# Kernel optimization log

Hardware: AMD Instinct MI355X
Metric: run time of the kernel (lower is better)

## Reference

```python
import jax, jax.numpy as jnp
import numpy as np

D_MODEL = 1472
N_HEADS = 6
D_KV = 64
INNER = N_HEADS * D_KV
NUM_BUCKETS = 32
MAX_DIST = 128


def _relative_position_bucket(relative_position, bidirectional=True,
                              num_buckets=NUM_BUCKETS, max_distance=MAX_DIST):
    ret = jnp.zeros_like(relative_position)
    if bidirectional:
        num_buckets //= 2
        ret = ret + (relative_position > 0).astype(jnp.int32) * num_buckets
        rel = jnp.abs(relative_position)
    else:
        rel = -jnp.minimum(relative_position, 0)
    max_exact = num_buckets // 2
    is_small = rel < max_exact
    rel_f = jnp.maximum(rel, 1).astype(jnp.float32)
    large = max_exact + (
        jnp.log(rel_f / max_exact) / np.log(max_distance / max_exact)
        * (num_buckets - max_exact)
    ).astype(jnp.int32)
    large = jnp.minimum(large, num_buckets - 1)
    return ret + jnp.where(is_small, rel, large)


def _position_bias(q_len, k_len, rel_bias):
    # rel_bias: [num_buckets, n_heads]
    ctx = jnp.arange(q_len)[:, None]
    mem = jnp.arange(k_len)[None, :]
    buckets = _relative_position_bucket(mem - ctx, bidirectional=True)
    values = rel_bias[buckets]                 # [Q, K, H]
    return jnp.transpose(values, (2, 0, 1))[None]  # [1, H, Q, K]


def setup_inputs() -> dict:
    key = jax.random.key(0)
    ks = jax.random.split(key, 8)
    B, S = 4, 2048
    scale = 0.02
    return {
        "kv_sequences": jax.random.normal(ks[0], (B, S, D_MODEL), jnp.float32),
        "q_sequences": jax.random.normal(ks[1], (B, S, D_MODEL), jnp.float32),
        "mask": jnp.zeros((B, 1, S, S), jnp.float32),
        "WQ": jax.random.normal(ks[2], (D_MODEL, INNER), jnp.float32) * scale,
        "WK": jax.random.normal(ks[3], (D_MODEL, INNER), jnp.float32) * scale,
        "WV": jax.random.normal(ks[4], (D_MODEL, INNER), jnp.float32) * scale,
        "WO": jax.random.normal(ks[5], (INNER, D_MODEL), jnp.float32) * scale,
        "rel_bias": jax.random.normal(ks[6], (NUM_BUCKETS, N_HEADS), jnp.float32) * scale,
    }


def reference(kv_sequences, q_sequences, mask, WQ, WK, WV, WO, rel_bias):
    B, Kl, _ = kv_sequences.shape
    Ql = q_sequences.shape[1]
    # projections -> [B, H, L, d_kv]
    q = (q_sequences @ WQ).reshape(B, Ql, N_HEADS, D_KV).transpose(0, 2, 1, 3)
    k = (kv_sequences @ WK).reshape(B, Kl, N_HEADS, D_KV).transpose(0, 2, 1, 3)
    v = (kv_sequences @ WV).reshape(B, Kl, N_HEADS, D_KV).transpose(0, 2, 1, 3)
    # T5-style: no 1/sqrt(d) scaling
    logits = jnp.einsum("bhqd,bhkd->bhqk", q, k)
    logits = logits + _position_bias(Ql, Kl, rel_bias)
    logits = logits + mask
    attn = jax.nn.softmax(logits.astype(jnp.float32), axis=-1).astype(logits.dtype)
    out = jnp.einsum("bhqk,bhkd->bhqd", attn, v)
    out = out.transpose(0, 2, 1, 3).reshape(B, Ql, INNER)
    return out @ WO
```

## Files before the change

### kernel.cpp

```cpp
#include <hip/hip_runtime.h>
#include <hip/hip_fp16.h>
#include <cstdint>

#define DM    1472
#define NH    6
#define DKV   64
#define INNER 384
#define BATCH 4
#define SEQ   2048
#define LOG2E 1.4426950408889634f

typedef __attribute__((ext_vector_type(8))) _Float16 half8;
typedef __attribute__((ext_vector_type(4))) _Float16 half4;
typedef __attribute__((ext_vector_type(4))) float f32x4;

__device__ __forceinline__ int swz64(int row, int b)  { return b ^ (((row >> 1) & 3) << 4); }
__device__ __forceinline__ int swz128(int row, int b) { return b ^ ((row & 7) << 4); }

__global__ void prep_weights(const float* __restrict__ WQ, const float* __restrict__ WK,
                             const float* __restrict__ WV, const float* __restrict__ WO,
                             _Float16* __restrict__ WqT, _Float16* __restrict__ WkT,
                             _Float16* __restrict__ WvT, _Float16* __restrict__ WoT) {
  int idx = blockIdx.x * blockDim.x + threadIdx.x;
  const int per = DM * INNER;
  if (idx >= 4 * per) return;
  int which = idx / per;
  int i = idx - which * per;
  if (which < 3) {
    const float* W = which == 0 ? WQ : (which == 1 ? WK : WV);
    _Float16* T = which == 0 ? WqT : (which == 1 ? WkT : WvT);
    int k = i / INNER, n = i - (i / INNER) * INNER;
    T[(size_t)n * DM + k] = (_Float16)W[i];
  } else {
    int k = i / DM, n = i - (i / DM) * DM;
    WoT[(size_t)n * INNER + k] = (_Float16)WO[i];
  }
}

__global__ void prep_bias(const float* __restrict__ rel_bias, float* __restrict__ biasS) {
  int idx = blockIdx.x * blockDim.x + threadIdx.x;
  const int TOT = NH * 4 * 4104;
  if (idx >= TOT) return;
  int h = idx / (4 * 4104);
  int rem = idx - h * 4 * 4104;
  int cc = rem / 4104;
  int i = rem - cc * 4104;
  int j = i + cc; if (j > 4094) j = 4094;
  int d = j - 2047;
  int ret = d > 0 ? 16 : 0;
  int a = d < 0 ? -d : d;
  int bucket;
  if (a < 8) bucket = ret + a;
  else {
    int large;
    if      (a >= 91) large = 15;
    else if (a >= 64) large = 14;
    else if (a >= 46) large = 13;
    else if (a >= 32) large = 12;
    else if (a >= 23) large = 11;
    else if (a >= 16) large = 10;
    else if (a >= 12) large = 9;
    else              large = 8;
    bucket = ret + large;
  }
  biasS[idx] = rel_bias[bucket * NH + h] * LOG2E;
}

__global__ __launch_bounds__(256) void proj_gemm(
    const float* __restrict__ Xq, const float* __restrict__ Xkv,
    const _Float16* __restrict__ WqT, const _Float16* __restrict__ WkT, const _Float16* __restrict__ WvT,
    _Float16* __restrict__ Qo, _Float16* __restrict__ Ko, _Float16* __restrict__ Vto) {
  const int z = blockIdx.z;
  const float* __restrict__ X = (z == 0) ? Xq : Xkv;
  const _Float16* __restrict__ WT = (z == 0) ? WqT : (z == 1 ? WkT : WvT);

  __shared__ alignas(16) _Float16 As[2][128 * 32];
  __shared__ alignas(16) _Float16 Bs[2][128 * 32];

  const int tid = threadIdx.x;
  const int lane = tid & 63, wave = tid >> 6;
  const int wm = wave >> 1, wn = wave & 1;
  const int bm = blockIdx.x, bn = blockIdx.y;
  const int l15 = lane & 15, lg = lane >> 4;

  f32x4 acc[4][4] = {};

  const int arow = tid >> 1, aseg = tid & 1;
  const int brow = tid >> 1, bseg = tid & 1;

  const float* asrc = X + (size_t)(bm * 128 + arow) * DM + aseg * 16;
  const _Float16* bsrc = WT + (size_t)(bn * 128 + brow) * DM + bseg * 16;

  const int NT = DM / 32;

  {
    f32x4 v0 = *(const f32x4*)(asrc);
    f32x4 v1 = *(const f32x4*)(asrc + 4);
    f32x4 v2 = *(const f32x4*)(asrc + 8);
    f32x4 v3 = *(const f32x4*)(asrc + 12);
    half8 b0 = *(const half8*)(bsrc);
    half8 b1 = *(const half8*)(bsrc + 8);
    half8 h0, h1;
#pragma unroll
    for (int j = 0; j < 4; ++j) {
      h0[j] = (_Float16)v0[j]; h0[4 + j] = (_Float16)v1[j];
      h1[j] = (_Float16)v2[j]; h1[4 + j] = (_Float16)v3[j];
    }
    char* AsW = (char*)&As[0][0];
    char* BsW = (char*)&Bs[0][0];
    *(half8*)(AsW + arow * 64 + swz64(arow, aseg * 32)) = h0;
    *(half8*)(AsW + arow * 64 + swz64(arow, aseg * 32 + 16)) = h1;
    *(half8*)(BsW + brow * 64 + swz64(brow, bseg * 32)) = b0;
    *(half8*)(BsW + brow * 64 + swz64(brow, bseg * 32 + 16)) = b1;
  }

  for (int t = 0; t < NT; ++t) {
    __syncthreads();
    const bool pre = (t + 1 < NT);
    f32x4 v0, v1, v2, v3;
    half8 nb0, nb1;
    if (pre) {
      const int kn = (t + 1) * 32;
      v0 = *(const f32x4*)(asrc + kn);
      v1 = *(const f32x4*)(asrc + kn + 4);
      v2 = *(const f32x4*)(asrc + kn + 8);
      v3 = *(const f32x4*)(asrc + kn + 12);
      nb0 = *(const half8*)(bsrc + kn);
      nb1 = *(const half8*)(bsrc + kn + 8);
    }

    const char* AsB = (const char*)&As[t & 1][0];
    const char* BsB = (const char*)&Bs[t & 1][0];
    half8 af[4], bf[4];
#pragma unroll
    for (int m = 0; m < 4; ++m) {
      int r = wm * 64 + m * 16 + l15;
      af[m] = *(const half8*)(AsB + r * 64 + swz64(r, lg * 16));
    }
#pragma unroll
    for (int n = 0; n < 4; ++n) {
      int r = wn * 64 + n * 16 + l15;
      bf[n] = *(const half8*)(BsB + r * 64 + swz64(r, lg * 16));
    }
    __builtin_amdgcn_s_setprio(1);
#pragma unroll
    for (int m = 0; m < 4; ++m)
#pragma unroll
      for (int n = 0; n < 4; ++n)
        acc[m][n] = __builtin_amdgcn_mfma_f32_16x16x32_f16(af[m], bf[n], acc[m][n], 0, 0, 0);
    __builtin_amdgcn_s_setprio(0);

    if (pre) {
      half8 h0, h1;
#pragma unroll
      for (int j = 0; j < 4; ++j) {
        h0[j] = (_Float16)v0[j]; h0[4 + j] = (_Float16)v1[j];
        h1[j] = (_Float16)v2[j]; h1[4 + j] = (_Float16)v3[j];
      }
      char* AsW = (char*)&As[(t + 1) & 1][0];
      char* BsW = (char*)&Bs[(t + 1) & 1][0];
      *(half8*)(AsW + arow * 64 + swz64(arow, aseg * 32)) = h0;
      *(half8*)(AsW + arow * 64 + swz64(arow, aseg * 32 + 16)) = h1;
      *(half8*)(BsW + brow * 64 + swz64(brow, bseg * 32)) = nb0;
      *(half8*)(BsW + brow * 64 + swz64(brow, bseg * 32 + 16)) = nb1;
    }
  }

#pragma unroll
  for (int m = 0; m < 4; ++m)
#pragma unroll
    for (int n = 0; n < 4; ++n)
#pragma unroll
      for (int r = 0; r < 4; ++r) {
        int gm = bm * 128 + wm * 64 + m * 16 + lg * 4 + r;
        int gn = bn * 128 + wn * 64 + n * 16 + l15;
        int b = gm >> 11, s = gm & 2047;
        int h = gn >> 6, dd = gn & 63;
        float av = acc[m][n][r];
        if (z == 0)      Qo[((size_t)(b * NH + h) * SEQ + s) * DKV + dd] = (_Float16)(av * LOG2E);
        else if (z == 1) Ko[((size_t)(b * NH + h) * SEQ + s) * DKV + dd] = (_Float16)av;
        else             Vto[((size_t)(b * NH + h) * DKV + dd) * SEQ + s] = (_Float16)av;
      }
}

__global__ __launch_bounds__(256) void attn_kernel(
    const _Float16* __restrict__ Q, const _Float16* __restrict__ K, const _Float16* __restrict__ Vt,
    const float* __restrict__ biasS, const float* __restrict__ mask, _Float16* __restrict__ AO) {
  const int bid = blockIdx.x;
  const int g = (bid & 7) * 96 + (bid >> 3);
  const int bh = g >> 5, qb = g & 31;
  const int b = bh / NH, h = bh - b * NH;
  const int q0 = qb * 64;
  const int tid = threadIdx.x, lane = tid & 63, wave = tid >> 6;
  const int l15 = lane & 15, lg = lane >> 4;

  __shared__ alignas(16) _Float16 Ks[2][64 * 64];
  __shared__ alignas(16) _Float16 Vs[2][64 * 64];
  __shared__ alignas(16) _Float16 Ps[4][16 * 72];

  const size_t bhS = (size_t)bh * SEQ;
  const int qq = q0 + wave * 16 + l15;

  const _Float16* Qbase = Q + (bhS + q0 + wave * 16) * DKV;
  half8 qf0 = *(const half8*)(Qbase + (size_t)l15 * DKV + lg * 8);
  half8 qf1 = *(const half8*)(Qbase + (size_t)l15 * DKV + 32 + lg * 8);

  const float* maskrow = mask + (size_t)b * SEQ * SEQ + (size_t)qq * SEQ;
  const int c = (3 - l15) & 3;
  const float* bptr[4];
#pragma unroll
  for (int nf = 0; nf < 4; ++nf)
    bptr[nf] = biasS + (size_t)(h * 4 + c) * 4104 + (nf * 16 + lg * 4 - qq + 2047 - c);

  float m_r = -1e30f, l_r = 0.f;
  f32x4 oacc[4] = {};

  const int srow = tid >> 2;
  const int scb = (tid & 3) * 32;
  const _Float16* Ksrc = K + (bhS + srow) * DKV + (scb >> 1);
  const _Float16* Vsrc = Vt + ((size_t)bh * DKV + srow) * SEQ + (scb >> 1);

  {
    half8 k0v = *(const half8*)(Ksrc);
    half8 k1v = *(const half8*)(Ksrc + 8);
    half8 v0v = *(const half8*)(Vsrc);
    half8 v1v = *(const half8*)(Vsrc + 8);
    char* KsW = (char*)&Ks[0][0];
    char* VsW = (char*)&Vs[0][0];
    *(half8*)(KsW + srow * 128 + swz128(srow, scb)) = k0v;
    *(half8*)(KsW + srow * 128 + swz128(srow, scb + 16)) = k1v;
    *(half8*)(VsW + srow * 128 + swz128(srow, scb)) = v0v;
    *(half8*)(VsW + srow * 128 + swz128(srow, scb + 16)) = v1v;
  }

  for (int t = 0; t < SEQ / 64; ++t) {
    __syncthreads();
    const int kt = t * 64;
    const bool pre = (t + 1 < SEQ / 64);
    half8 knA, knB, vnA, vnB;
    if (pre) {
      const _Float16* kp = Ksrc + (size_t)(kt + 64) * DKV;
      knA = *(const half8*)(kp);
      knB = *(const half8*)(kp + 8);
      const _Float16* vp = Vsrc + kt + 64;
      vnA = *(const half8*)(vp);
      vnB = *(const half8*)(vp + 8);
    }
    const char* KsB = (const char*)&Ks[t & 1][0];
    const char* VsB = (const char*)&Vs[t & 1][0];
    char* PsB = (char*)&Ps[wave][0];

    f32x4 sacc[4] = {};
    __builtin_amdgcn_s_setprio(1);
#pragma unroll
    for (int nf = 0; nf < 4; ++nf) {
      int kr = nf * 16 + l15;
      half8 kf0 = *(const half8*)(KsB + kr * 128 + swz128(kr, lg * 16));
      half8 kf1 = *(const half8*)(KsB + kr * 128 + swz128(kr, 64 + lg * 16));
      sacc[nf] = __builtin_amdgcn_mfma_f32_16x16x32_f16(kf0, qf0, sacc[nf], 0, 0, 0);
      sacc[nf] = __builtin_amdgcn_mfma_f32_16x16x32_f16(kf1, qf1, sacc[nf], 0, 0, 0);
    }
    __builtin_amdgcn_s_setprio(0);

    float sv[4][4];
    float mx = -1e30f;
#pragma unroll
    for (int nf = 0; nf < 4; ++nf) {
      f32x4 bv = *(const f32x4*)(bptr[nf] + kt);
      f32x4 mv = *(const f32x4*)(maskrow + kt + nf * 16 + lg * 4);
#pragma unroll
      for (int r = 0; r < 4; ++r) {
        float s = sacc[nf][r] + bv[r] + mv[r] * LOG2E;
        sv[nf][r] = s;
        mx = fmaxf(mx, s);
      }
    }
    mx = fmaxf(mx, __shfl_xor(mx, 16));
    mx = fmaxf(mx, __shfl_xor(mx, 32));
    const float mnew = fmaxf(m_r, mx);
    const float sc_ = __builtin_amdgcn_exp2f(m_r - mnew);
    float rs = 0.f;
#pragma unroll
    for (int nf = 0; nf < 4; ++nf) {
      half4 ph;
#pragma unroll
      for (int r = 0; r < 4; ++r) {
        float p = __builtin_amdgcn_exp2f(sv[nf][r] - mnew);
        rs += p;
        ph[r] = (_Float16)p;
      }
      *(half4*)(PsB + l15 * 144 + nf * 32 + lg * 8) = ph;
    }
    rs += __shfl_xor(rs, 16);
    rs += __shfl_xor(rs, 32);
    l_r = l_r * sc_ + rs;
    m_r = mnew;

    f32x4 scv;
#pragma unroll
    for (int r = 0; r < 4; ++r) scv[r] = __shfl(sc_, lg * 4 + r);
#pragma unroll
    for (int df = 0; df < 4; ++df) oacc[df] *= scv;

    __builtin_amdgcn_s_setprio(1);
#pragma unroll
    for (int ks = 0; ks < 2; ++ks) {
      half8 pa = *(const half8*)(PsB + l15 * 144 + ks * 64 + lg * 16);
#pragma unroll
      for (int df = 0; df < 4; ++df) {
        int vr = df * 16 + l15;
        half8 vb = *(const half8*)(VsB + vr * 128 + swz128(vr, ks * 64 + lg * 16));
        oacc[df] = __builtin_amdgcn_mfma_f32_16x16x32_f16(pa, vb, oacc[df], 0, 0, 0);
      }
    }
    __builtin_amdgcn_s_setprio(0);

    if (pre) {
      char* KsW = (char*)&Ks[(t + 1) & 1][0];
      char* VsW = (char*)&Vs[(t + 1) & 1][0];
      *(half8*)(KsW + srow * 128 + swz128(srow, scb)) = knA;
      *(half8*)(KsW + srow * 128 + swz128(srow, scb + 16)) = knB;
      *(half8*)(VsW + srow * 128 + swz128(srow, scb)) = vnA;
      *(half8*)(VsW + srow * 128 + swz128(srow, scb + 16)) = vnB;
    }
  }

  f32x4 lv;
#pragma unroll
  for (int r = 0; r < 4; ++r) lv[r] = __shfl(l_r, lg * 4 + r);
#pragma unroll
  for (int df = 0; df < 4; ++df) {
    int dd = df * 16 + l15;
#pragma unroll
    for (int r = 0; r < 4; ++r) {
      int qrow = q0 + wave * 16 + lg * 4 + r;
      AO[((size_t)(b * SEQ + qrow)) * INNER + h * DKV + dd] = (_Float16)(oacc[df][r] / lv[r]);
    }
  }
}

__global__ __launch_bounds__(256) void out_gemm(
    const _Float16* __restrict__ A, const _Float16* __restrict__ BT, float* __restrict__ C) {
  __shared__ alignas(16) _Float16 As[2][128 * 32];
  __shared__ alignas(16) _Float16 Bs[2][64 * 32];

  const int tid = threadIdx.x, lane = tid & 63, wave = tid >> 6;
  const int wm = wave >> 1, wn = wave & 1;
  const int bm = blockIdx.x, bn = blockIdx.y;
  const int l15 = lane & 15, lg = lane >> 4;

  f32x4 acc[4][2] = {};
  const int arow = tid >> 1, aseg = tid & 1;
  const int brow = tid >> 2, bchunk = tid & 3;
  const _Float16* asrc = A + (size_t)(bm * 128 + arow) * INNER + aseg * 16;
  const _Float16* bsrc = BT + (size_t)(bn * 64 + brow) * INNER + bchunk * 8;

  const int NT = INNER / 32;

  {
    half8 a0 = *(const half8*)(asrc);
    half8 a1 = *(const half8*)(asrc + 8);
    half8 b0 = *(const half8*)(bsrc);
    char* AsW = (char*)&As[0][0];
    char* BsW = (char*)&Bs[0][0];
    *(half8*)(AsW + arow * 64 + swz64(arow, aseg * 32)) = a0;
    *(half8*)(AsW + arow * 64 + swz64(arow, aseg * 32 + 16)) = a1;
    *(half8*)(BsW + brow * 64 + swz64(brow, bchunk * 16)) = b0;
  }

  for (int t = 0; t < NT; ++t) {
    __syncthreads();
    const bool pre = (t + 1 < NT);
    half8 na0, na1, nb0;
    if (pre) {
      const int kn = (t + 1) * 32;
      na0 = *(const half8*)(asrc + kn);
      na1 = *(const half8*)(asrc + kn + 8);
      nb0 = *(const half8*)(bsrc + kn);
    }

    const char* AsB = (const char*)&As[t & 1][0];
    const char* BsB = (const char*)&Bs[t & 1][0];
    half8 af[4], bf[2];
#pragma unroll
    for (int m = 0; m < 4; ++m) {
      int r = wm * 64 + m * 16 + l15;
      af[m] = *(const half8*)(AsB + r * 64 + swz64(r, lg * 16));
    }
#pragma unroll
    for (int n = 0; n < 2; ++n) {
      int r = wn * 32 + n * 16 + l15;
      bf[n] = *(const half8*)(BsB + r * 64 + swz64(r, lg * 16));
    }
    __builtin_amdgcn_s_setprio(1);
#pragma unroll
    for (int m = 0; m < 4; ++m)
#pragma unroll
      for (int n = 0; n < 2; ++n)
        acc[m][n] = __builtin_amdgcn_mfma_f32_16x16x32_f16(af[m], bf[n], acc[m][n], 0, 0, 0);
    __builtin_amdgcn_s_setprio(0);

    if (pre) {
      char* AsW = (char*)&As[(t + 1) & 1][0];
      char* BsW = (char*)&Bs[(t + 1) & 1][0];
      *(half8*)(AsW + arow * 64 + swz64(arow, aseg * 32)) = na0;
      *(half8*)(AsW + arow * 64 + swz64(arow, aseg * 32 + 16)) = na1;
      *(half8*)(BsW + brow * 64 + swz64(brow, bchunk * 16)) = nb0;
    }
  }

#pragma unroll
  for (int m = 0; m < 4; ++m)
#pragma unroll
    for (int n = 0; n < 2; ++n)
#pragma unroll
      for (int r = 0; r < 4; ++r) {
        int gm = bm * 128 + wm * 64 + m * 16 + lg * 4 + r;
        int gn = bn * 64 + wn * 32 + n * 16 + l15;
        C[(size_t)gm * DM + gn] = acc[m][n][r];
      }
}

extern "C" void kernel_launch(void* const* d_in, const int* in_sizes, int n_in,
                              void* d_out, int out_size, void* d_ws, size_t ws_size,
                              hipStream_t stream) {
  const float* kv   = (const float*)d_in[0];
  const float* qs   = (const float*)d_in[1];
  const float* mask = (const float*)d_in[2];
  const float* WQ   = (const float*)d_in[3];
  const float* WK   = (const float*)d_in[4];
  const float* WV   = (const float*)d_in[5];
  const float* WO   = (const float*)d_in[6];
  const float* rb   = (const float*)d_in[7];
  float* out = (float*)d_out;
  char* ws = (char*)d_ws;

  const size_t WT_BYTES  = (size_t)INNER * DM * 2;
  const size_t QKV_BYTES = (size_t)BATCH * NH * SEQ * DKV * 2;
  _Float16* WqT = (_Float16*)(ws);
  _Float16* WkT = (_Float16*)(ws + WT_BYTES);
  _Float16* WvT = (_Float16*)(ws + 2 * WT_BYTES);
  _Float16* WoT = (_Float16*)(ws + 3 * WT_BYTES);
  _Float16* Qh  = (_Float16*)(ws + 4 * WT_BYTES);
  _Float16* Kh  = (_Float16*)(ws + 4 * WT_BYTES + QKV_BYTES);
  _Float16* Vth = (_Float16*)(ws + 4 * WT_BYTES + 2 * QKV_BYTES);
  _Float16* AO  = (_Float16*)(ws + 4 * WT_BYTES + 3 * QKV_BYTES);
  float* biasS  = (float*)(ws + 4 * WT_BYTES + 4 * QKV_BYTES);

  hipLaunchKernelGGL(prep_weights, dim3((4 * DM * INNER + 255) / 256), dim3(256), 0, stream,
                     WQ, WK, WV, WO, WqT, WkT, WvT, WoT);
  hipLaunchKernelGGL(prep_bias, dim3((NH * 4 * 4104 + 255) / 256), dim3(256), 0, stream, rb, biasS);
  hipLaunchKernelGGL(proj_gemm, dim3(64, 3, 3), dim3(256), 0, stream,
                     qs, kv, WqT, WkT, WvT, Qh, Kh, Vth);
  hipLaunchKernelGGL(attn_kernel, dim3(768), dim3(256), 0, stream,
                     Qh, Kh, Vth, biasS, mask, AO);
  hipLaunchKernelGGL(out_gemm, dim3(64, 23), dim3(256), 0, stream, AO, WoT, out);
}
```

Baseline: 209.7 us.

## Use direct global-to-LDS loads in projection GEMM with fp32 A tile

The projection GEMM now stages the fp32 activation tile and the fp16 weight tile into shared memory with global_load_lds 16-byte direct loads. This replaces the register-staged load, convert and store path, with swizzled layouts computed on the source address side. The fp16 conversion of the activations moves to after the shared-memory read. K and V weights are addressed as one contiguous concatenated matrix, relying on WkT and WvT being adjacent in the workspace. Shared memory for the A tile doubles, which may reduce occupancy, and each block now does more conversion work per tile.

```diff
diff --git a/kernel.cpp b/kernel.cpp
--- a/kernel.cpp
+++ b/kernel.cpp
@@ -16,6 +16,11 @@
 
 __device__ __forceinline__ int swz64(int row, int b)  { return b ^ (((row >> 1) & 3) << 4); }
 __device__ __forceinline__ int swz128(int row, int b) { return b ^ ((row & 7) << 4); }
+
+__device__ __forceinline__ void gload16(const void* g, const void* l) {
+  __builtin_amdgcn_global_load_lds((const __attribute__((address_space(1))) void*)g,
+                                   (__attribute__((address_space(3))) void*)l, 16, 0, 0);
+}
 
 __global__ void prep_weights(const float* __restrict__ WQ, const float* __restrict__ WK,
                              const float* __restrict__ WV, const float* __restrict__ WO,
@@ -68,80 +73,77 @@
 
 __global__ __launch_bounds__(256) void proj_gemm(
     const float* __restrict__ Xq, const float* __restrict__ Xkv,
-    const _Float16* __restrict__ WqT, const _Float16* __restrict__ WkT, const _Float16* __restrict__ WvT,
+    const _Float16* __restrict__ WqT, const _Float16* __restrict__ WkvT,
     _Float16* __restrict__ Qo, _Float16* __restrict__ Ko, _Float16* __restrict__ Vto) {
-  const int z = blockIdx.z;
-  const float* __restrict__ X = (z == 0) ? Xq : Xkv;
-  const _Float16* __restrict__ WT = (z == 0) ? WqT : (z == 1 ? WkT : WvT);
-
-  __shared__ alignas(16) _Float16 As[2][128 * 32];
+  const int bm = blockIdx.x, by = blockIdx.y;
+  const bool isQ = by < 3;
+  const float* __restrict__ X = isQ ? Xq : Xkv;
+  const _Float16* __restrict__ WT = isQ ? (WqT + (size_t)by * 128 * DM)
+                                        : (WkvT + (size_t)(by - 3) * 128 * DM);
+
+  __shared__ alignas(16) float    As[2][128 * 32];
   __shared__ alignas(16) _Float16 Bs[2][128 * 32];
 
   const int tid = threadIdx.x;
   const int lane = tid & 63, wave = tid >> 6;
   const int wm = wave >> 1, wn = wave & 1;
-  const int bm = blockIdx.x, bn = blockIdx.y;
   const int l15 = lane & 15, lg = lane >> 4;
 
   f32x4 acc[4][4] = {};
 
-  const int arow = tid >> 1, aseg = tid & 1;
-  const int brow = tid >> 1, bseg = tid & 1;
-
-  const float* asrc = X + (size_t)(bm * 128 + arow) * DM + aseg * 16;
-  const _Float16* bsrc = WT + (size_t)(bn * 128 + brow) * DM + bseg * 16;
+  const int aoff = 4 * ((lane & 7) ^ (lane >> 3));
+  const float* asrc[4];
+#pragma unroll
+  for (int c = 0; c < 4; ++c)
+    asrc[c] = X + (size_t)(bm * 128 + (wave * 4 + c) * 8 + (lane >> 3)) * DM + aoff;
+  const int boff = 8 * ((lane & 3) ^ ((lane >> 3) & 3));
+  const _Float16* bsrc[2];
+#pragma unroll
+  for (int c = 0; c < 2; ++c)
+    bsrc[c] = WT + (size_t)((wave * 2 + c) * 16 + (lane >> 2)) * DM + boff;
 
   const int NT = DM / 32;
 
-  {
-    f32x4 v0 = *(const f32x4*)(asrc);
-    f32x4 v1 = *(const f32x4*)(asrc + 4);
-    f32x4 v2 = *(const f32x4*)(asrc + 8);
-    f32x4 v3 = *(const f32x4*)(asrc + 12);
-    half8 b0 = *(const half8*)(bsrc);
-    half8 b1 = *(const half8*)(bsrc + 8);
-    half8 h0, h1;
-#pragma unroll
-    for (int j = 0; j < 4; ++j) {
-      h0[j] = (_Float16)v0[j]; h0[4 + j] = (_Float16)v1[j];
-      h1[j] = (_Float16)v2[j]; h1[4 + j] = (_Float16)v3[j];
-    }
-    char* AsW = (char*)&As[0][0];
-    char* BsW = (char*)&Bs[0][0];
-    *(half8*)(AsW + arow * 64 + swz64(arow, aseg * 32)) = h0;
-    *(half8*)(AsW + arow * 64 + swz64(arow, aseg * 32 + 16)) = h1;
-    *(half8*)(BsW + brow * 64 + swz64(brow, bseg * 32)) = b0;
-    *(half8*)(BsW + brow * 64 + swz64(brow, bseg * 32 + 16)) = b1;
-  }
+#pragma unroll
+  for (int c = 0; c < 4; ++c)
+    gload16(asrc[c], (const char*)&As[0][0] + (wave * 4 + c) * 1024);
+#pragma unroll
+  for (int c = 0; c < 2; ++c)
+    gload16(bsrc[c], (const char*)&Bs[0][0] + (wave * 2 + c) * 1024);
+  __syncthreads();
 
   for (int t = 0; t < NT; ++t) {
-    __syncthreads();
-    const bool pre = (t + 1 < NT);
-    f32x4 v0, v1, v2, v3;
-    half8 nb0, nb1;
-    if (pre) {
-      const int kn = (t + 1) * 32;
-      v0 = *(const f32x4*)(asrc + kn);
-      v1 = *(const f32x4*)(asrc + kn + 4);
-      v2 = *(const f32x4*)(asrc + kn + 8);
-      v3 = *(const f32x4*)(asrc + kn + 12);
-      nb0 = *(const half8*)(bsrc + kn);
-      nb1 = *(const half8*)(bsrc + kn + 8);
-    }
-
-    const char* AsB = (const char*)&As[t & 1][0];
-    const char* BsB = (const char*)&Bs[t & 1][0];
+    if (t + 1 < NT) {
+      const int nb = (t + 1) & 1;
+      const int kf = (t + 1) * 32;
+#pragma unroll
+      for (int c = 0; c < 4; ++c)
+        gload16(asrc[c] + kf, (const char*)&As[nb][0] + (wave * 4 + c) * 1024);
+#pragma unroll
+      for (int c = 0; c < 2; ++c)
+        gload16(bsrc[c] + kf, (const char*)&Bs[nb][0] + (wave * 2 + c) * 1024);
+    }
+
+    const char* Ab = (const char*)&As[t & 1][0];
+    const char* Bb = (const char*)&Bs[t & 1][0];
     half8 af[4], bf[4];
 #pragma unroll
     for (int m = 0; m < 4; ++m) {
       int r = wm * 64 + m * 16 + l15;
-      af[m] = *(const half8*)(AsB + r * 64 + swz64(r, lg * 16));
+      int s = (r & 7) << 4;
+      f32x4 x0 = *(const f32x4*)(Ab + r * 128 + ((lg * 32) ^ s));
+      f32x4 x1 = *(const f32x4*)(Ab + r * 128 + ((lg * 32 + 16) ^ s));
+      half8 h;
+#pragma unroll
+      for (int j = 0; j < 4; ++j) { h[j] = (_Float16)x0[j]; h[4 + j] = (_Float16)x1[j]; }
+      af[m] = h;
     }
 #pragma unroll
     for (int n = 0; n < 4; ++n) {
       int r = wn * 64 + n * 16 + l15;
-      bf[n] = *(const half8*)(BsB + r * 64 + swz64(r, lg * 16));
-    }
+      bf[n] = *(const half8*)(Bb + r * 64 + ((lg * 16) ^ (((r >> 1) & 3) << 4)));
+    }
+
     __builtin_amdgcn_s_setprio(1);
 #pragma unroll
     for (int m = 0; m < 4; ++m)
@@ -150,20 +152,7 @@
         acc[m][n] = __builtin_amdgcn_mfma_f32_16x16x32_f16(af[m], bf[n], acc[m][n], 0, 0, 0);
     __builtin_amdgcn_s_setprio(0);
 
-    if (pre) {
-      half8 h0, h1;
-#pragma unroll
-      for (int j = 0; j < 4; ++j) {
-        h0[j] = (_Float16)v0[j]; h0[4 + j] = (_Float16)v1[j];
-        h1[j] = (_Float16)v2[j]; h1[4 + j] = (_Float16)v3[j];
-      }
-      char* AsW = (char*)&As[(t + 1) & 1][0];
-      char* BsW = (char*)&Bs[(t + 1) & 1][0];
-      *(half8*)(AsW + arow * 64 + swz64(arow, aseg * 32)) = h0;
-      *(half8*)(AsW + arow * 64 + swz64(arow, aseg * 32 + 16)) = h1;
-      *(half8*)(BsW + brow * 64 + swz64(brow, bseg * 32)) = nb0;
-      *(half8*)(BsW + brow * 64 + swz64(brow, bseg * 32 + 16)) = nb1;
-    }
+    __syncthreads();
   }
 
 #pragma unroll
@@ -173,13 +162,24 @@
 #pragma unroll
       for (int r = 0; r < 4; ++r) {
         int gm = bm * 128 + wm * 64 + m * 16 + lg * 4 + r;
-        int gn = bn * 128 + wn * 64 + n * 16 + l15;
+        int gnl = wn * 64 + n * 16 + l15;
         int b = gm >> 11, s = gm & 2047;
-        int h = gn >> 6, dd = gn & 63;
         float av = acc[m][n][r];
-        if (z == 0)      Qo[((size_t)(b * NH + h) * SEQ + s) * DKV + dd] = (_Float16)(av * LOG2E);
-        else if (z == 1) Ko[((size_t)(b * NH + h) * SEQ + s) * DKV + dd] = (_Float16)av;
-        else             Vto[((size_t)(b * NH + h) * DKV + dd) * SEQ + s] = (_Float16)av;
+        if (isQ) {
+          int gn = by * 128 + gnl;
+          int h = gn >> 6, dd = gn & 63;
+          Qo[((size_t)(b * NH + h) * SEQ + s) * DKV + dd] = (_Float16)(av * LOG2E);
+        } else {
+          int gn = (by - 3) * 128 + gnl;
+          if (gn < INNER) {
+            int h = gn >> 6, dd = gn & 63;
+            Ko[((size_t)(b * NH + h) * SEQ + s) * DKV + dd] = (_Float16)av;
+          } else {
+            int gnv = gn - INNER;
+            int h = gnv >> 6, dd = gnv & 63;
+            Vto[((size_t)(b * NH + h) * DKV + dd) * SEQ + s] = (_Float16)av;
+          }
+        }
       }
 }
 
@@ -450,8 +450,8 @@
   hipLaunchKernelGGL(prep_weights, dim3((4 * DM * INNER + 255) / 256), dim3(256), 0, stream,
                      WQ, WK, WV, WO, WqT, WkT, WvT, WoT);
   hipLaunchKernelGGL(prep_bias, dim3((NH * 4 * 4104 + 255) / 256), dim3(256), 0, stream, rb, biasS);
-  hipLaunchKernelGGL(proj_gemm, dim3(64, 3, 3), dim3(256), 0, stream,
-                     qs, kv, WqT, WkT, WvT, Qh, Kh, Vth);
+  hipLaunchKernelGGL(proj_gemm, dim3(64, 9), dim3(256), 0, stream,
+                     qs, kv, WqT, WkT, Qh, Kh, Vth);
   hipLaunchKernelGGL(attn_kernel, dim3(768), dim3(256), 0, stream,
                      Qh, Kh, Vth, biasS, mask, AO);
   hipLaunchKernelGGL(out_gemm, dim3(64, 23), dim3(256), 0, stream, AO, WoT, out);
```

New measurement: 194.6 us. 7.2% less time.
